# Optimization experiments

Hardware: AMD Instinct MI355X
Metric: run time of the kernel (lower is better)

Reference implementation:

```python
import jax, jax.numpy as jnp
import numpy as np

N = 50000          # num_assets / nodes
E = 1_600_000      # edges (avg degree 32)
F = 128            # num_features
R = 4              # num_relations
H = 1              # heads
O1, O2 = 15, 10    # RGATConv out_channels (hard-coded in module)
NEG_SLOPE = 0.2    # leaky_relu slope in RGATConv
BN_EPS = 1e-5


def setup_inputs() -> dict:
    key = jax.random.key(0)
    ks = jax.random.split(key, 24)
    s = 0.1
    return {
        "node_emb": jax.random.normal(ks[0], (N, F), jnp.float32),
        "edge_index": jax.random.randint(ks[1], (2, E), 0, N),
        "edge_types": jax.random.randint(ks[2], (E,), 0, R),
        "edge_attr": jax.random.normal(ks[3], (E, 1), jnp.float32),
        # RGATConv layer 1 params
        "W1": jax.random.normal(ks[4], (R, F, H * O1), jnp.float32) * s,
        "q1": jax.random.normal(ks[5], (H * O1, H), jnp.float32) * s,
        "k1": jax.random.normal(ks[6], (H * O1, H), jnp.float32) * s,
        "e1": jax.random.normal(ks[7], (H * O1, H), jnp.float32) * s,
        "We1": jax.random.normal(ks[8], (1, H * O1), jnp.float32) * s,  # lin_edge
        "b1": jax.random.normal(ks[9], (H * O1,), jnp.float32) * s,
        # RGATConv layer 2 params
        "W2": jax.random.normal(ks[10], (R, H * O1, H * O2), jnp.float32) * s,
        "q2": jax.random.normal(ks[11], (H * O2, H), jnp.float32) * s,
        "k2": jax.random.normal(ks[12], (H * O2, H), jnp.float32) * s,
        "e2": jax.random.normal(ks[13], (H * O2, H), jnp.float32) * s,
        "We2": jax.random.normal(ks[14], (1, H * O2), jnp.float32) * s,
        "b2": jax.random.normal(ks[15], (O2,), jnp.float32) * s,
        # BatchNorm affine params
        "g1": 1.0 + jax.random.normal(ks[16], (H * O1,), jnp.float32) * 0.05,
        "beta1": jax.random.normal(ks[17], (H * O1,), jnp.float32) * 0.05,
        "g2": 1.0 + jax.random.normal(ks[18], (O2,), jnp.float32) * 0.05,
        "beta2": jax.random.normal(ks[19], (O2,), jnp.float32) * 0.05,
        # head Linear(10, 1)
        "w_head": jax.random.normal(ks[20], (O2, 1), jnp.float32) * s,
        "b_head": jax.random.normal(ks[21], (1,), jnp.float32) * s,
    }


def _segment_softmax(alpha, dst, n):
    amax = jax.ops.segment_max(alpha, dst, num_segments=n)
    ex = jnp.exp(alpha - amax[dst])
    denom = jax.ops.segment_sum(ex, dst, num_segments=n)
    return ex / (denom[dst] + 1e-16)


def _rgat(x, src, dst, etype, eattr, W, q, k, e, We, b, heads, out_ch, concat):
    n = x.shape[0]
    # per-relation transform of all nodes, then gather per-edge (same math as
    # PyG's per-edge bmm with W[edge_type])
    xt = jnp.einsum('nf,rfo->nro', x, W)            # [N, R, H*O]
    out_i = xt[dst, etype]                          # [E, H*O] (target)
    out_j = xt[src, etype]                          # [E, H*O] (source)
    alpha = out_i @ q + out_j @ k + (eattr @ We) @ e  # [E, H]
    alpha = jax.nn.leaky_relu(alpha, NEG_SLOPE)
    alpha = _segment_softmax(alpha, dst, n)          # across-relation softmax over dst
    msg = (alpha[:, :, None] * out_j.reshape(-1, heads, out_ch)).reshape(-1, heads * out_ch)
    agg = jax.ops.segment_sum(msg, dst, num_segments=n)
    if not concat:
        agg = agg.reshape(n, heads, out_ch).mean(axis=1)
    return agg + b


def _bn_elu(x, g, beta):
    # training-mode BatchNorm1d (batch statistics, biased variance) + ELU
    mu = x.mean(axis=0)
    var = x.var(axis=0)
    xh = (x - mu) / jnp.sqrt(var + BN_EPS)
    return jax.nn.elu(xh * g + beta)


def reference(node_emb, edge_index, edge_types, edge_attr,
              W1, q1, k1, e1, We1, b1,
              W2, q2, k2, e2, We2, b2,
              g1, beta1, g2, beta2, w_head, b_head):
    src, dst = edge_index[0], edge_index[1]
    x = _rgat(node_emb, src, dst, edge_types, edge_attr,
              W1, q1, k1, e1, We1, b1, H, O1, True)
    x = _bn_elu(x, g1, beta1)
    x = _rgat(x, src, dst, edge_types, edge_attr,
              W2, q2, k2, e2, We2, b2, H, O2, False)
    x = _bn_elu(x, g2, beta2)
    return x @ w_head + b_head                       # [N, 1]
```

## Files before the change

kernel.cpp:

```cpp
#include <hip/hip_runtime.h>


typedef unsigned short ushort_t;
typedef unsigned int uint_t;
typedef __attribute__((ext_vector_type(8))) short bf16x8;
typedef __attribute__((ext_vector_type(4))) float f32x4;

#define NEG_SLOPE 0.2f
#define BN_EPS 1e-5f
#define NBUCK 512

__device__ __forceinline__ float bf2f(ushort_t u) {
    return __uint_as_float(((uint_t)u) << 16);
}
__device__ __forceinline__ ushort_t f2bf(float f) {
    uint_t x = __float_as_uint(f);
    x += 0x7FFFu + ((x >> 16) & 1u);
    return (ushort_t)(x >> 16);
}
__device__ __forceinline__ float loadf(const void* p, int i, int isb) {
    return isb ? bf2f(((const ushort_t*)p)[i]) : ((const float*)p)[i];
}

__global__ __launch_bounds__(256) void k_prep(const uint_t* __restrict__ x,
                                              const void* __restrict__ W1,
                                              const void* __restrict__ W2,
                                              const void* __restrict__ q1b,
                                              const void* __restrict__ k1b,
                                              int* __restrict__ dflag,
                                              int* __restrict__ bcur,
                                              float* __restrict__ stats1,
                                              float* __restrict__ stats2,
                                              ushort_t* __restrict__ Wsw,
                                              float* __restrict__ Wf2, int cap) {
    __shared__ int cnt;
    int t = threadIdx.x;
    if (t == 0) cnt = 0;
    __syncthreads();
    uint_t u = x[t * 37];
    uint_t lo_exp = (u >> 7) & 0xFF;
    atomicAdd(&cnt, (lo_exp >= 96 && lo_exp <= 150) ? 1 : 0);
    __syncthreads();
    int isb = (cnt > 192) ? 1 : 0;
    if (blockIdx.x == 0) {
        if (t == 0) dflag[0] = isb;
        for (int i = t; i < NBUCK; i += 256) bcur[i] = i * cap;
        stats1[t] = 0.f;
        stats2[t] = 0.f;
        for (int idx = t; idx < 15 * 40; idx += 256) {
            int f = idx / 40, j = idx % 40, r = j / 10, o = j % 10;
            Wf2[idx] = loadf(W2, (r * 15 + f) * 10 + o, isb);
        }
    }
    for (int idx = blockIdx.x * 256 + t; idx < 20 * 64 * 8; idx += gridDim.x * 256) {
        int j = idx & 7, lane = (idx >> 3) & 63, fr = idx >> 9;
        int ks = fr / 5, ct = fr % 5;
        int k = ks * 32 + (lane >> 4) * 8 + j;
        int c = ct * 16 + (lane & 15);
        float v = 0.f;
        if (c < 64) {
            int r = c >> 4, o = c & 15;
            if (o < 15) v = loadf(W1, (r * 128 + k) * 15 + o, isb);
        } else if (c < 72) {
            int r = (c - 64) & 3;
            const void* vec = (c < 68) ? q1b : k1b;
            float s = 0.f;
#pragma unroll
            for (int o = 0; o < 15; ++o)
                s += loadf(W1, (r * 128 + k) * 15 + o, isb) * loadf(vec, o, isb);
            v = s;
        }
        Wsw[idx] = f2bf(v);
    }
}

__global__ __launch_bounds__(512) void k_bucket(const int* __restrict__ ei,
                                                const int* __restrict__ et,
                                                const void* __restrict__ ea,
                                                const int* __restrict__ flag,
                                                int* __restrict__ bcur,
                                                int2* __restrict__ tmp,
                                                int E, int npb) {
    extern __shared__ int2 srec[];
    __shared__ int cnt[NBUCK];
    __shared__ int lofs[NBUCK + 1];
    __shared__ int gpos[NBUCK];
    int t = threadIdx.x;
    int isb = flag[0];
    cnt[t] = 0;
    __syncthreads();
    int e0 = blockIdx.x * 8192;
    for (int i = 0; i < 16; ++i) {
        int e = e0 + i * 512 + t;
        if (e < E) atomicAdd(&cnt[ei[E + e] / npb], 1);
    }
    __syncthreads();
    int myc = cnt[t];
    for (int off = 1; off < NBUCK; off <<= 1) {
        int v = (t >= off) ? cnt[t - off] : 0;
        __syncthreads();
        cnt[t] += v;
        __syncthreads();
    }
    lofs[t] = cnt[t] - myc;
    if (t == NBUCK - 1) lofs[NBUCK] = cnt[NBUCK - 1];
    __syncthreads();
    cnt[t] = lofs[t];
    __syncthreads();
    for (int i = 0; i < 16; ++i) {
        int e = e0 + i * 512 + t;
        if (e < E) {
            int d = ei[E + e];
            int b = d / npb;
            int ldst = d - b * npb;
            int idx = atomicAdd(&cnt[b], 1);
            int2 r;
            r.x = (int)((uint_t)ei[e] | ((uint_t)et[e] << 23) | ((uint_t)ldst << 25));
            r.y = __float_as_int(loadf(ea, e, isb));
            srec[idx] = r;
        }
    }
    __syncthreads();
    int c_b = lofs[t + 1] - lofs[t];
    gpos[t] = atomicAdd(&bcur[t], c_b);
    __syncthreads();
    int total = lofs[NBUCK];
    for (int i = t; i < total; i += 512) {
        int lo = 0, hi = NBUCK - 1;
        while (lo < hi) {
            int mid = (lo + hi + 1) >> 1;
            if (lofs[mid] <= i) lo = mid; else hi = mid - 1;
        }
        tmp[gpos[lo] + (i - lofs[lo])] = srec[i];
    }
}

__global__ __launch_bounds__(256) void k_b2csr(const int2* __restrict__ tmp,
                                               const int* __restrict__ bcur,
                                               int* __restrict__ rs,
                                               int* __restrict__ re,
                                               int2* __restrict__ ebuf,
                                               int N, int npb, int cap) {
    __shared__ int cnt[128];
    __shared__ int lofs[129];
    int b = blockIdx.x, t = threadIdx.x;
    int s0 = b * cap;
    int s1 = bcur[b];
    if (t < 128) cnt[t] = 0;
    __syncthreads();
    for (int p = s0 + t; p < s1; p += 256) {
        uint_t x = (uint_t)tmp[p].x;
        atomicAdd(&cnt[(x >> 25) & 0x7F], 1);
    }
    __syncthreads();
    int myc = (t < 128) ? cnt[t] : 0;
    for (int off = 1; off < 128; off <<= 1) {
        int v = (t >= off && t < 128) ? cnt[t - off] : 0;
        __syncthreads();
        if (t < 128) cnt[t] += v;
        __syncthreads();
    }
    if (t < 128) {
        lofs[t] = cnt[t] - myc;
        if (t == 127) lofs[128] = cnt[127];
    }
    __syncthreads();
    int node0 = b * npb;
    if (t < npb && node0 + t < N) {
        rs[node0 + t] = s0 + lofs[t];
        re[node0 + t] = s0 + lofs[t + 1];
    }
    if (t < 128) cnt[t] = lofs[t];
    __syncthreads();
    for (int p = s0 + t; p < s1; p += 256) {
        int2 r = tmp[p];
        uint_t x = (uint_t)r.x;
        int ldst = (x >> 25) & 0x7F;
        int idx = atomicAdd(&cnt[ldst], 1);
        int2 o;
        o.x = (int)(x & 0x7FFFFF) | (((int)(x >> 23) & 3) << 20);
        o.y = (int)(((uint_t)(node0 + ldst) << 16) |
                    (uint_t)f2bf(__int_as_float(r.y)));
        ebuf[s0 + idx] = o;
    }
}

__global__ __launch_bounds__(256) void k_t1(const void* __restrict__ xin,
                                            const ushort_t* __restrict__ Wsw,
                                            const int* __restrict__ flag,
                                            ushort_t* __restrict__ xt,
                                            float* __restrict__ dq,
                                            float* __restrict__ dk,
                                            int N, int ntiles, int nwaves) {
    int isb = flag[0];
    int lane = threadIdx.x & 63;
    int gw = blockIdx.x * 4 + (threadIdx.x >> 6);
    bf16x8 bfr[20];
    const uint4* wq = (const uint4*)Wsw;
#pragma unroll
    for (int fr = 0; fr < 20; ++fr)
        bfr[fr] = __builtin_bit_cast(bf16x8, wq[fr * 64 + lane]);
    int row = lane & 15, quad = lane >> 4;
    for (int tile = gw; tile < ntiles; tile += nwaves) {
        int n0 = tile * 16;
        f32x4 acc[5];
#pragma unroll
        for (int ct = 0; ct < 5; ++ct) acc[ct] = (f32x4){0.f, 0.f, 0.f, 0.f};
        int nA = n0 + row;
        if (nA >= N) nA = N - 1;
#pragma unroll
        for (int ks = 0; ks < 4; ++ks) {
            bf16x8 af;
            if (isb) {
                uint4 u = *(const uint4*)((const ushort_t*)xin + (size_t)nA * 128 + ks * 32 + quad * 8);
                af = __builtin_bit_cast(bf16x8, u);
            } else {
                const float* xf = (const float*)xin + (size_t)nA * 128 + ks * 32 + quad * 8;
#pragma unroll
                for (int j = 0; j < 8; ++j) af[j] = (short)f2bf(xf[j]);
            }
#pragma unroll
            for (int ct = 0; ct < 5; ++ct)
                acc[ct] = __builtin_amdgcn_mfma_f32_16x16x32_bf16(af, bfr[ks * 5 + ct], acc[ct], 0, 0, 0);
        }
#pragma unroll
        for (int i = 0; i < 4; ++i) {
            int n = n0 + quad * 4 + i;
            if (n < N) {
#pragma unroll
                for (int ct = 0; ct < 4; ++ct)
                    xt[(size_t)n * 64 + ct * 16 + row] = f2bf(acc[ct][i]);
                if (row < 4) dq[n * 4 + row] = acc[4][i];
                else if (row < 8) dk[n * 4 + (row - 4)] = acc[4][i];
            }
        }
    }
}

__global__ __launch_bounds__(256) void k_t2(const float* __restrict__ in,
                                            const float* __restrict__ stats,
                                            const void* __restrict__ g,
                                            const void* __restrict__ beta,
                                            const float* __restrict__ Wf,
                                            const void* __restrict__ qb,
                                            const void* __restrict__ kb,
                                            const int* __restrict__ flag,
                                            ushort_t* __restrict__ xt,
                                            float* __restrict__ dq,
                                            float* __restrict__ dk, int N) {
    int isb = flag[0];
    int t = threadIdx.x;
    int lane = t & 63;
    int r = t >> 6;
    int n = blockIdx.x * 64 + lane;
    if (n >= N) return;
    float invN = 1.f / (float)N;
    float v[15];
#pragma unroll
    for (int c = 0; c < 15; ++c) {
        float mean = stats[c * 16] * invN;
        float var = stats[c * 16 + 8] * invN - mean * mean;
        float inv = rsqrtf(var + BN_EPS);
        float h = (in[(size_t)n * 15 + c] - mean) * inv * loadf(g, c, isb) + loadf(beta, c, isb);
        v[c] = h > 0.f ? h : expm1f(h);
    }
    float acc[10];
#pragma unroll
    for (int o = 0; o < 10; ++o) acc[o] = 0.f;
#pragma unroll
    for (int f = 0; f < 15; ++f) {
        const float* wp = Wf + f * 40 + r * 10;
#pragma unroll
        for (int o = 0; o < 10; ++o) acc[o] += v[f] * wp[o];
    }
    float a = 0.f, b = 0.f;
#pragma unroll
    for (int o = 0; o < 10; ++o) {
        a += acc[o] * loadf(qb, o, isb);
        b += acc[o] * loadf(kb, o, isb);
    }
    dq[n * 4 + r] = a;
    dk[n * 4 + r] = b;
    ushort_t* xr = xt + (size_t)n * 64 + r * 16;
    uint_t pk[8];
#pragma unroll
    for (int j = 0; j < 5; ++j)
        pk[j] = (uint_t)f2bf(acc[2 * j]) | ((uint_t)f2bf(acc[2 * j + 1]) << 16);
    pk[5] = 0; pk[6] = 0; pk[7] = 0;
    *(uint4*)(xr)     = make_uint4(pk[0], pk[1], pk[2], pk[3]);
    *(uint4*)(xr + 8) = make_uint4(pk[4], pk[5], pk[6], pk[7]);
}

template <int O>
__global__ __launch_bounds__(256) void k_alpha(const int2* __restrict__ ebuf,
                                               const float* __restrict__ dq,
                                               const float* __restrict__ dk,
                                               const void* __restrict__ Web,
                                               const void* __restrict__ eb,
                                               const int* __restrict__ flag,
                                               int2* __restrict__ ab2, int Etot) {
    int isb = flag[0];
    float c = 0.f;
#pragma unroll
    for (int o = 0; o < O; ++o) c += loadf(Web, o, isb) * loadf(eb, o, isb);
    int e = blockIdx.x * 256 + threadIdx.x;
    if (e >= Etot) return;
    int2 rec = ebuf[e];
    int sr = rec.x & 0xFFFFF, et = rec.x >> 20;
    uint_t y = (uint_t)rec.y;
    int dst = (int)(y >> 16);
    float ea = bf2f((ushort_t)(y & 0xFFFFu));
    float a = dq[dst * 4 + et] + dk[sr * 4 + et] + c * ea;
    a = a > 0.f ? a : NEG_SLOPE * a;
    ab2[e] = make_int2(__float_as_int(__expf(a)), rec.x);
}

template <int O>
__global__ __launch_bounds__(256) void k_gather(const int* __restrict__ rs,
                                                const int* __restrict__ re,
                                                const int2* __restrict__ ab2,
                                                const ushort_t* __restrict__ xt,
                                                const void* __restrict__ bb,
                                                const int* __restrict__ flag,
                                                float* __restrict__ out, int N) {
    int isb = flag[0];
    int lane = threadIdx.x & 63;
    int w = threadIdx.x >> 6;
    int n = blockIdx.x * 4 + w;
    if (n >= N) return;
    int start = rs[n], end = re[n];
    int g = lane >> 4, ch = lane & 15;
    float acc = 0.f, s = 0.f;
    int p = start + g;
    for (; p + 12 < end; p += 16) {
        int2 v0 = ab2[p];
        int2 v1 = ab2[p + 4];
        int2 v2 = ab2[p + 8];
        int2 v3 = ab2[p + 12];
        float x0 = bf2f(xt[(size_t)((v0.y & 0xFFFFF) * 4 + (v0.y >> 20)) * 16 + ch]);
        float x1 = bf2f(xt[(size_t)((v1.y & 0xFFFFF) * 4 + (v1.y >> 20)) * 16 + ch]);
        float x2 = bf2f(xt[(size_t)((v2.y & 0xFFFFF) * 4 + (v2.y >> 20)) * 16 + ch]);
        float x3 = bf2f(xt[(size_t)((v3.y & 0xFFFFF) * 4 + (v3.y >> 20)) * 16 + ch]);
        float e0 = __int_as_float(v0.x), e1 = __int_as_float(v1.x);
        float e2 = __int_as_float(v2.x), e3 = __int_as_float(v3.x);
        s += (e0 + e1) + (e2 + e3);
        acc += e0 * x0;
        acc += e1 * x1;
        acc += e2 * x2;
        acc += e3 * x3;
    }
    for (; p < end; p += 4) {
        int2 v = ab2[p];
        float e = __int_as_float(v.x);
        acc += e * bf2f(xt[(size_t)((v.y & 0xFFFFF) * 4 + (v.y >> 20)) * 16 + ch]);
        s += e;
    }
    s   += __shfl_xor(s, 16, 64);
    s   += __shfl_xor(s, 32, 64);
    acc += __shfl_xor(acc, 16, 64);
    acc += __shfl_xor(acc, 32, 64);
    if (lane < O) out[(size_t)n * O + lane] = acc / (s + 1e-16f) + loadf(bb, lane, isb);
}

template <int C>
__global__ __launch_bounds__(256) void k_bnstats(const float* __restrict__ in,
                                                 float* __restrict__ S, int N) {
    int t = threadIdx.x;
    int ch = t & 15, rg = t >> 4;
    float s1 = 0.f, s2 = 0.f;
    int row0 = blockIdx.x * 256;
    int rowEnd = row0 + 256;
    if (rowEnd > N) rowEnd = N;
    if (ch < C) {
        for (int r = row0 + rg; r < rowEnd; r += 16) {
            float v = in[(size_t)r * C + ch];
            s1 += v;
            s2 += v * v;
        }
    }
    __shared__ float L1[256], L2[256];
    L1[t] = s1; L2[t] = s2;
    __syncthreads();
    for (int k = 128; k >= 16; k >>= 1) {
        if (t < k) { L1[t] += L1[t + k]; L2[t] += L2[t + k]; }
        __syncthreads();
    }
    if (t < C) {
        atomicAdd(&S[t * 16], L1[t]);
        atomicAdd(&S[t * 16 + 8], L2[t]);
    }
}

__global__ __launch_bounds__(256) void k_head(const float* __restrict__ in,
                                              const float* __restrict__ stats,
                                              const void* __restrict__ g,
                                              const void* __restrict__ beta,
                                              const void* __restrict__ wh,
                                              const void* __restrict__ bh,
                                              const int* __restrict__ flag,
                                              void* __restrict__ out, int N) {
    int isb = flag[0];
    int n = blockIdx.x * 256 + threadIdx.x;
    if (n >= N) return;
    float invN = 1.f / (float)N;
    float r = loadf(bh, 0, isb);
#pragma unroll
    for (int c = 0; c < 10; ++c) {
        float mean = stats[c * 16] * invN;
        float var = stats[c * 16 + 8] * invN - mean * mean;
        float inv = rsqrtf(var + BN_EPS);
        float h = (in[(size_t)n * 10 + c] - mean) * inv * loadf(g, c, isb) + loadf(beta, c, isb);
        float e = h > 0.f ? h : expm1f(h);
        r += e * loadf(wh, c, isb);
    }
    if (isb) ((ushort_t*)out)[n] = f2bf(r);
    else     ((float*)out)[n] = r;
}

extern "C" void kernel_launch(void* const* d_in, const int* in_sizes, int n_in,
                              void* d_out, int out_size, void* d_ws, size_t ws_size,
                              hipStream_t stream) {
    const void* node_emb  = d_in[0];
    const int*  edge_index = (const int*)d_in[1];
    const int*  edge_types = (const int*)d_in[2];
    const void* edge_attr = d_in[3];
    const void* W1  = d_in[4];
    const void* q1  = d_in[5];
    const void* k1  = d_in[6];
    const void* e1  = d_in[7];
    const void* We1 = d_in[8];
    const void* b1  = d_in[9];
    const void* W2  = d_in[10];
    const void* q2  = d_in[11];
    const void* k2  = d_in[12];
    const void* e2  = d_in[13];
    const void* We2 = d_in[14];
    const void* b2  = d_in[15];
    const void* g1  = d_in[16];
    const void* beta1 = d_in[17];
    const void* g2  = d_in[18];
    const void* beta2 = d_in[19];
    const void* w_head = d_in[20];
    const void* b_head = d_in[21];

    int N = in_sizes[0] / 128;
    int E = in_sizes[1] / 2;
    int npb = (N + NBUCK - 1) / NBUCK;
    int nbuck = (N + npb - 1) / npb;
    int cap = E / nbuck + 512;
    size_t slots = (size_t)nbuck * cap;

    char* ws = (char*)d_ws;
    size_t off = 0;
    auto alloc = [&](size_t bytes) -> void* {
        void* p = ws + off;
        off = (off + bytes + 255) & ~(size_t)255;
        return p;
    };
    int*   rs      = (int*)alloc((size_t)N * 4);
    int*   re      = (int*)alloc((size_t)N * 4);
    int*   bcur    = (int*)alloc((NBUCK) * 4);
    int*   dflag   = (int*)alloc(256);
    int2*  ebuf    = (int2*)alloc(slots * 8);
    int2*  ab2     = (int2*)alloc(slots * 8);
    size_t big = (size_t)N * 64 * 2;
    if (slots * 8 > big) big = slots * 8;
    ushort_t* xt1  = (ushort_t*)alloc(big);
    int2*  etmp    = (int2*)xt1;
    float* dq1     = (float*)alloc((size_t)N * 16);
    float* dk1     = (float*)alloc((size_t)N * 16);
    float* out1    = (float*)alloc((size_t)N * 15 * 4);
    float* stats1  = (float*)alloc(256 * 4);
    float* stats2  = (float*)alloc(256 * 4);
    ushort_t* Wsw  = (ushort_t*)alloc(20 * 64 * 8 * 2);
    float* Wf2     = (float*)alloc(600 * 4);
    ushort_t* xt2 = xt1;
    float* dq2  = dq1;
    float* dk2  = dk1;
    float* out2 = out1;

    int NB_N = (N + 255) / 256;
    int NB_T2 = (N + 63) / 64;
    int NB_G = (N + 3) / 4;
    int NB_A = (int)((slots + 255) / 256);
    int NB_B = (E + 8191) / 8192;
    int ntiles = (N + 15) / 16;
    int NB_T1 = 391;
    int nwaves = NB_T1 * 4;

    k_prep<<<40, 256, 0, stream>>>((const uint_t*)node_emb, W1, W2, q1, k1,
                                   dflag, bcur, stats1, stats2, Wsw, Wf2, cap);
    k_bucket<<<NB_B, 512, 8192 * sizeof(int2), stream>>>(edge_index, edge_types, edge_attr,
                                                         dflag, bcur, etmp, E, npb);
    k_b2csr<<<nbuck, 256, 0, stream>>>(etmp, bcur, rs, re, ebuf, N, npb, cap);

    k_t1<<<NB_T1, 256, 0, stream>>>(node_emb, Wsw, dflag, xt1, dq1, dk1, N, ntiles, nwaves);
    k_alpha<15><<<NB_A, 256, 0, stream>>>(ebuf, dq1, dk1, We1, e1, dflag, ab2, (int)slots);
    k_gather<15><<<NB_G, 256, 0, stream>>>(rs, re, ab2, xt1, b1, dflag, out1, N);
    k_bnstats<15><<<NB_N, 256, 0, stream>>>(out1, stats1, N);
    k_t2<<<NB_T2, 256, 0, stream>>>(out1, stats1, g1, beta1, Wf2, q2, k2, dflag, xt2, dq2, dk2, N);
    k_alpha<10><<<NB_A, 256, 0, stream>>>(ebuf, dq2, dk2, We2, e2, dflag, ab2, (int)slots);
    k_gather<10><<<NB_G, 256, 0, stream>>>(rs, re, ab2, xt2, b2, dflag, out2, N);
    k_bnstats<10><<<NB_N, 256, 0, stream>>>(out2, stats2, N);
    k_head<<<NB_N, 256, 0, stream>>>(out2, stats2, g2, beta2, w_head, b_head, dflag, d_out, N);
}
```

Measured before the change: 335.3 us.

## Fuse layer-1 attention logits into CSR build and reorder transform before bucketing

Moves the layer-1 node transform ahead of edge bucketing so its per-node attention terms are ready when the CSR build runs. The CSR kernel then computes each edge's leaky-relu exp logit and writes it straight into the attention buffer, removing the separate layer-1 alpha pass over all edge slots. This needs a dedicated buffer for the temporary bucket edges rather than aliasing the transform output, which costs extra workspace memory. The CSR build now does random gathers of dq and dk per edge.

```diff
diff --git a/kernel.cpp b/kernel.cpp
--- a/kernel.cpp
+++ b/kernel.cpp
@@ -137,13 +137,23 @@
 
 __global__ __launch_bounds__(256) void k_b2csr(const int2* __restrict__ tmp,
                                                const int* __restrict__ bcur,
+                                               const float* __restrict__ dq,
+                                               const float* __restrict__ dk,
+                                               const void* __restrict__ Web,
+                                               const void* __restrict__ eb,
+                                               const int* __restrict__ flag,
                                                int* __restrict__ rs,
                                                int* __restrict__ re,
                                                int2* __restrict__ ebuf,
+                                               int2* __restrict__ ab2,
                                                int N, int npb, int cap) {
     __shared__ int cnt[128];
     __shared__ int lofs[129];
     int b = blockIdx.x, t = threadIdx.x;
+    int isb = flag[0];
+    float cw = 0.f;
+#pragma unroll
+    for (int o = 0; o < 15; ++o) cw += loadf(Web, o, isb) * loadf(eb, o, isb);
     int s0 = b * cap;
     int s1 = bcur[b];
     if (t < 128) cnt[t] = 0;
@@ -177,11 +187,18 @@
         uint_t x = (uint_t)r.x;
         int ldst = (x >> 25) & 0x7F;
         int idx = atomicAdd(&cnt[ldst], 1);
+        int sr = (int)(x & 0x7FFFFF);
+        int et = (int)(x >> 23) & 3;
+        int dst = node0 + ldst;
+        float ea = __int_as_float(r.y);
+        int packed = sr | (et << 20);
         int2 o;
-        o.x = (int)(x & 0x7FFFFF) | (((int)(x >> 23) & 3) << 20);
-        o.y = (int)(((uint_t)(node0 + ldst) << 16) |
-                    (uint_t)f2bf(__int_as_float(r.y)));
+        o.x = packed;
+        o.y = (int)(((uint_t)dst << 16) | (uint_t)f2bf(ea));
         ebuf[s0 + idx] = o;
+        float a = dq[dst * 4 + et] + dk[sr * 4 + et] + cw * ea;
+        a = a > 0.f ? a : NEG_SLOPE * a;
+        ab2[s0 + idx] = make_int2(__float_as_int(__expf(a)), packed);
     }
 }
 
@@ -463,10 +480,8 @@
     int*   dflag   = (int*)alloc(256);
     int2*  ebuf    = (int2*)alloc(slots * 8);
     int2*  ab2     = (int2*)alloc(slots * 8);
-    size_t big = (size_t)N * 64 * 2;
-    if (slots * 8 > big) big = slots * 8;
-    ushort_t* xt1  = (ushort_t*)alloc(big);
-    int2*  etmp    = (int2*)xt1;
+    int2*  etmp    = (int2*)alloc(slots * 8);
+    ushort_t* xt1  = (ushort_t*)alloc((size_t)N * 64 * 2);
     float* dq1     = (float*)alloc((size_t)N * 16);
     float* dk1     = (float*)alloc((size_t)N * 16);
     float* out1    = (float*)alloc((size_t)N * 15 * 4);
@@ -490,12 +505,11 @@
 
     k_prep<<<40, 256, 0, stream>>>((const uint_t*)node_emb, W1, W2, q1, k1,
                                    dflag, bcur, stats1, stats2, Wsw, Wf2, cap);
+    k_t1<<<NB_T1, 256, 0, stream>>>(node_emb, Wsw, dflag, xt1, dq1, dk1, N, ntiles, nwaves);
     k_bucket<<<NB_B, 512, 8192 * sizeof(int2), stream>>>(edge_index, edge_types, edge_attr,
                                                          dflag, bcur, etmp, E, npb);
-    k_b2csr<<<nbuck, 256, 0, stream>>>(etmp, bcur, rs, re, ebuf, N, npb, cap);
-
-    k_t1<<<NB_T1, 256, 0, stream>>>(node_emb, Wsw, dflag, xt1, dq1, dk1, N, ntiles, nwaves);
-    k_alpha<15><<<NB_A, 256, 0, stream>>>(ebuf, dq1, dk1, We1, e1, dflag, ab2, (int)slots);
+    k_b2csr<<<nbuck, 256, 0, stream>>>(etmp, bcur, dq1, dk1, We1, e1, dflag,
+                                       rs, re, ebuf, ab2, N, npb, cap);
     k_gather<15><<<NB_G, 256, 0, stream>>>(rs, re, ab2, xt1, b1, dflag, out1, N);
     k_bnstats<15><<<NB_N, 256, 0, stream>>>(out1, stats1, N);
     k_t2<<<NB_T2, 256, 0, stream>>>(out1, stats1, g1, beta1, Wf2, q2, k2, dflag, xt2, dq2, dk2, N);
```

New measurement: 340.7 us. About the same (+1.6%).
